# Performance work log

Hardware: AMD Instinct MI355X
Metric: run time of the kernel (lower is better)

Reference implementation:

```python
import jax, jax.numpy as jnp
import numpy as np
from jax import lax

T, I, H = 8192, 1024, 1024


def setup_inputs() -> dict:
    key = jax.random.key(0)
    ks = jax.random.split(key, 7)
    s = 1.0 / np.sqrt(H)
    x = jax.random.normal(ks[0], (T, I), dtype=jnp.float32)
    W_ih = jax.random.uniform(ks[1], (4 * H, I), minval=-s, maxval=s, dtype=jnp.float32)
    W_hh = jax.random.uniform(ks[2], (4 * H, H), minval=-s, maxval=s, dtype=jnp.float32)
    b_ih = jax.random.uniform(ks[3], (4 * H,), minval=-s, maxval=s, dtype=jnp.float32)
    b_hh = jax.random.uniform(ks[4], (4 * H,), minval=-s, maxval=s, dtype=jnp.float32)
    h0 = jax.random.normal(ks[5], (H,), dtype=jnp.float32)
    c0 = jax.random.uniform(ks[6], (H,), dtype=jnp.float32)
    return {"x": x, "W_ih": W_ih, "W_hh": W_hh, "b_ih": b_ih, "b_hh": b_hh, "h0": h0, "c0": c0}


def reference(x, W_ih, W_hh, b_ih, b_hh, h0, c0):
    # Precompute the input contribution to all gates in one big GEMM: [T, 4H]
    gates_x = x @ W_ih.T + (b_ih + b_hh)

    def step(carry, gx):
        h, c = carry
        g = gx + h @ W_hh.T  # [4H]
        i, f, gc, o = jnp.split(g, 4)  # PyTorch gate order: input, forget, cell, output
        i = jax.nn.sigmoid(i)
        f = jax.nn.sigmoid(f)
        gc = jnp.tanh(gc)
        o = jax.nn.sigmoid(o)
        c_new = f * c + i * gc
        h_new = o * jnp.tanh(c_new)
        return (h_new, c_new), h_new

    (_, _), hs = lax.scan(step, (h0, c0), gates_x)
    return hs  # [T, H] — the per-timestep outputs collected in fullDataOutput
```

## Files before the change

### kernel.cpp

```cpp
#include <hip/hip_runtime.h>
#include <cstdint>

#define T_STEPS 8192
#define HDIM 1024

__device__ __forceinline__ float dot4(float4 a, float4 b) {
    return a.x * b.x + a.y * b.y + a.z * b.z + a.w * b.w;
}
__device__ __forceinline__ float sigmoidf_(float x) {
    return 1.0f / (1.0f + __expf(-x));
}
__device__ __forceinline__ float tanhf_(float x) {
    return 1.0f - 2.0f / (__expf(2.0f * x) + 1.0f);
}

__global__ __launch_bounds__(256, 1)
void lstm_persistent(const float* __restrict__ x,
                     const float* __restrict__ W_ih,
                     const float* __restrict__ W_hh,
                     const float* __restrict__ b_ih,
                     const float* __restrict__ b_hh,
                     const float* __restrict__ h0,
                     const float* __restrict__ c0,
                     float* __restrict__ out,
                     unsigned long long* __restrict__ ring)
{
    __shared__ float h_lds[2][HDIM];

    const int tid = threadIdx.x;
    const int w   = tid >> 6;
    const int l   = tid & 63;
    const int u   = blockIdx.x * 4 + w;

    float4 Whh[4][4], Wih[4][4];
#pragma unroll
    for (int q = 0; q < 4; ++q) {
        const float* rh = W_hh + (size_t)(q * HDIM + u) * HDIM;
        const float* ri = W_ih + (size_t)(q * HDIM + u) * HDIM;
#pragma unroll
        for (int i = 0; i < 4; ++i) {
            Whh[q][i] = *(const float4*)(rh + 4 * l + 256 * i);
            Wih[q][i] = *(const float4*)(ri + 4 * l + 256 * i);
        }
    }
    float bias[4];
#pragma unroll
    for (int q = 0; q < 4; ++q) bias[q] = b_ih[q * HDIM + u] + b_hh[q * HDIM + u];
    float c = c0[u];

    float4 hr[4];
#pragma unroll
    for (int i = 0; i < 4; ++i) hr[i] = *(const float4*)(h0 + 4 * l + 256 * i);

    float4 xr[4], xn[4];
#pragma unroll
    for (int i = 0; i < 4; ++i) xr[i] = *(const float4*)(x + 4 * l + 256 * i);
    float gxp[4];
#pragma unroll
    for (int q = 0; q < 4; ++q) {
        float a = 0.f;
#pragma unroll
        for (int i = 0; i < 4; ++i) a += dot4(Wih[q][i], xr[i]);
        gxp[q] = a;
    }
#pragma unroll
    for (int i = 0; i < 4; ++i) xr[i] = *(const float4*)(x + HDIM + 4 * l + 256 * i);

    for (int t = 0; t < T_STEPS; ++t) {
        float acc[4];
#pragma unroll
        for (int q = 0; q < 4; ++q) {
            float a = gxp[q];
#pragma unroll
            for (int i = 0; i < 4; ++i) a += dot4(Whh[q][i], hr[i]);
            acc[q] = a;
        }
#pragma unroll
        for (int m = 1; m < 64; m <<= 1) {
#pragma unroll
            for (int q = 0; q < 4; ++q) acc[q] += __shfl_xor(acc[q], m, 64);
        }
        const float gi = sigmoidf_(acc[0] + bias[0]);
        const float gf = sigmoidf_(acc[1] + bias[1]);
        const float gg = tanhf_   (acc[2] + bias[2]);
        const float go = sigmoidf_(acc[3] + bias[3]);
        c = gf * c + gi * gg;
        const float hval = go * tanhf_(c);

        if (l == 0) {
            out[(size_t)t * HDIM + u] = hval;
            const unsigned long long pk =
                ((unsigned long long)(unsigned)(t + 1) << 32) |
                (unsigned long long)__float_as_uint(hval);
            __hip_atomic_store(&ring[(t & 1) * HDIM + u], pk,
                               __ATOMIC_RELAXED, __HIP_MEMORY_SCOPE_AGENT);
        }
        if (t == T_STEPS - 1) break;

        {
            const int tn = (t + 2 < T_STEPS) ? (t + 2) : (T_STEPS - 1);
            const float* xp = x + (size_t)tn * HDIM;
#pragma unroll
            for (int i = 0; i < 4; ++i) xn[i] = *(const float4*)(xp + 4 * l + 256 * i);
        }
#pragma unroll
        for (int q = 0; q < 4; ++q) {
            float a = 0.f;
#pragma unroll
            for (int i = 0; i < 4; ++i) a += dot4(Wih[q][i], xr[i]);
            gxp[q] = a;
        }

        {
            const unsigned e = (unsigned)(t + 1);
            const unsigned long long* rp = ring + (t & 1) * HDIM + tid;
            unsigned long long v0, v1, v2, v3;
            for (;;) {
                v0 = __hip_atomic_load(rp,       __ATOMIC_RELAXED, __HIP_MEMORY_SCOPE_AGENT);
                v1 = __hip_atomic_load(rp + 256, __ATOMIC_RELAXED, __HIP_MEMORY_SCOPE_AGENT);
                v2 = __hip_atomic_load(rp + 512, __ATOMIC_RELAXED, __HIP_MEMORY_SCOPE_AGENT);
                v3 = __hip_atomic_load(rp + 768, __ATOMIC_RELAXED, __HIP_MEMORY_SCOPE_AGENT);
                if ((unsigned)(v0 >> 32) == e && (unsigned)(v1 >> 32) == e &&
                    (unsigned)(v2 >> 32) == e && (unsigned)(v3 >> 32) == e) break;
                __builtin_amdgcn_s_sleep(1);
            }
            const int ns = (t + 1) & 1;
            h_lds[ns][tid      ] = __uint_as_float((unsigned)v0);
            h_lds[ns][tid + 256] = __uint_as_float((unsigned)v1);
            h_lds[ns][tid + 512] = __uint_as_float((unsigned)v2);
            h_lds[ns][tid + 768] = __uint_as_float((unsigned)v3);
        }
        __syncthreads();
        {
            const int ns = (t + 1) & 1;
#pragma unroll
            for (int i = 0; i < 4; ++i)
                hr[i] = *(const float4*)&h_lds[ns][4 * l + 256 * i];
        }
#pragma unroll
        for (int i = 0; i < 4; ++i) xr[i] = xn[i];
    }
}

extern "C" void kernel_launch(void* const* d_in, const int* in_sizes, int n_in,
                              void* d_out, int out_size, void* d_ws, size_t ws_size,
                              hipStream_t stream)
{
    const float* x    = (const float*)d_in[0];
    const float* W_ih = (const float*)d_in[1];
    const float* W_hh = (const float*)d_in[2];
    const float* b_ih = (const float*)d_in[3];
    const float* b_hh = (const float*)d_in[4];
    const float* h0   = (const float*)d_in[5];
    const float* c0   = (const float*)d_in[6];

    unsigned long long* ring = (unsigned long long*)d_ws;
    hipMemsetAsync(d_ws, 0, 2 * HDIM * sizeof(unsigned long long), stream);
    lstm_persistent<<<256, 256, 0, stream>>>(x, W_ih, W_hh, b_ih, b_hh, h0, c0,
                                             (float*)d_out, ring);
}
```

Measured before the change: 23.61 ms.

## Halve block count, widen blocks, and poll ring with 16-byte uncached loads

The grid goes from 256 blocks of 256 threads to 128 blocks of 512 threads, so each block owns 8 hidden units and fewer blocks take part in the per-step cross-block handshake. The spin-wait now uses one inline-asm global_load_dwordx4 with sc0 sc1 cache bypass per thread, covering two ring entries, instead of four 8-byte atomic loads. The s_sleep backoff is dropped, and the h output store now comes after the ring publish. The risks are heavier memory traffic from tight polling and a 16-byte read of two 8-byte entries that is not guaranteed atomic as a whole, although each entry carries its own step tag.

New measurement: 25.82 ms. 9.4% more time.

```diff
diff --git a/kernel.cpp b/kernel.cpp
--- a/kernel.cpp
+++ b/kernel.cpp
@@ -2,19 +2,27 @@
 #include <cstdint>
 
 #define T_STEPS 8192
-#define HDIM 1024
+#define HDIM    1024
+#define NBLK    128
+#define NTHR    512
+
+typedef unsigned int u32x4 __attribute__((ext_vector_type(4)));
 
 __device__ __forceinline__ float dot4(float4 a, float4 b) {
     return a.x * b.x + a.y * b.y + a.z * b.z + a.w * b.w;
 }
-__device__ __forceinline__ float sigmoidf_(float x) {
-    return 1.0f / (1.0f + __expf(-x));
-}
-__device__ __forceinline__ float tanhf_(float x) {
-    return 1.0f - 2.0f / (__expf(2.0f * x) + 1.0f);
+__device__ __forceinline__ float sigmoidf_(float v) { return 1.0f / (1.0f + __expf(-v)); }
+__device__ __forceinline__ float tanhf_(float v)    { return 1.0f - 2.0f / (__expf(2.0f * v) + 1.0f); }
+
+__device__ __forceinline__ u32x4 poll2(unsigned long long a) {
+    u32x4 r;
+    asm volatile("global_load_dwordx4 %0, %1, off sc0 sc1\n\t"
+                 "s_waitcnt vmcnt(0)"
+                 : "=&v"(r) : "v"(a) : "memory");
+    return r;
 }
 
-__global__ __launch_bounds__(256, 1)
+__global__ __launch_bounds__(NTHR, 2)
 void lstm_persistent(const float* __restrict__ x,
                      const float* __restrict__ W_ih,
                      const float* __restrict__ W_hh,
@@ -30,7 +38,7 @@
     const int tid = threadIdx.x;
     const int w   = tid >> 6;
     const int l   = tid & 63;
-    const int u   = blockIdx.x * 4 + w;
+    const int u   = (blockIdx.x << 3) + w;
 
     float4 Whh[4][4], Wih[4][4];
 #pragma unroll
@@ -52,17 +60,20 @@
 #pragma unroll
     for (int i = 0; i < 4; ++i) hr[i] = *(const float4*)(h0 + 4 * l + 256 * i);
 
+    float gxp[4];
+    {
+        float4 x0[4];
+#pragma unroll
+        for (int i = 0; i < 4; ++i) x0[i] = *(const float4*)(x + 4 * l + 256 * i);
+#pragma unroll
+        for (int q = 0; q < 4; ++q) {
+            float a = 0.f;
+#pragma unroll
+            for (int i = 0; i < 4; ++i) a += dot4(Wih[q][i], x0[i]);
+            gxp[q] = a;
+        }
+    }
     float4 xr[4], xn[4];
-#pragma unroll
-    for (int i = 0; i < 4; ++i) xr[i] = *(const float4*)(x + 4 * l + 256 * i);
-    float gxp[4];
-#pragma unroll
-    for (int q = 0; q < 4; ++q) {
-        float a = 0.f;
-#pragma unroll
-        for (int i = 0; i < 4; ++i) a += dot4(Wih[q][i], xr[i]);
-        gxp[q] = a;
-    }
 #pragma unroll
     for (int i = 0; i < 4; ++i) xr[i] = *(const float4*)(x + HDIM + 4 * l + 256 * i);
 
@@ -88,12 +99,12 @@
         const float hval = go * tanhf_(c);
 
         if (l == 0) {
-            out[(size_t)t * HDIM + u] = hval;
             const unsigned long long pk =
                 ((unsigned long long)(unsigned)(t + 1) << 32) |
                 (unsigned long long)__float_as_uint(hval);
             __hip_atomic_store(&ring[(t & 1) * HDIM + u], pk,
                                __ATOMIC_RELAXED, __HIP_MEMORY_SCOPE_AGENT);
+            out[(size_t)t * HDIM + u] = hval;
         }
         if (t == T_STEPS - 1) break;
 
@@ -113,22 +124,16 @@
 
         {
             const unsigned e = (unsigned)(t + 1);
-            const unsigned long long* rp = ring + (t & 1) * HDIM + tid;
-            unsigned long long v0, v1, v2, v3;
+            const unsigned long long base =
+                (unsigned long long)(ring + (t & 1) * HDIM + 2 * tid);
+            u32x4 p;
             for (;;) {
-                v0 = __hip_atomic_load(rp,       __ATOMIC_RELAXED, __HIP_MEMORY_SCOPE_AGENT);
-                v1 = __hip_atomic_load(rp + 256, __ATOMIC_RELAXED, __HIP_MEMORY_SCOPE_AGENT);
-                v2 = __hip_atomic_load(rp + 512, __ATOMIC_RELAXED, __HIP_MEMORY_SCOPE_AGENT);
-                v3 = __hip_atomic_load(rp + 768, __ATOMIC_RELAXED, __HIP_MEMORY_SCOPE_AGENT);
-                if ((unsigned)(v0 >> 32) == e && (unsigned)(v1 >> 32) == e &&
-                    (unsigned)(v2 >> 32) == e && (unsigned)(v3 >> 32) == e) break;
-                __builtin_amdgcn_s_sleep(1);
+                p = poll2(base);
+                if ((unsigned)p.y == e && (unsigned)p.w == e) break;
             }
             const int ns = (t + 1) & 1;
-            h_lds[ns][tid      ] = __uint_as_float((unsigned)v0);
-            h_lds[ns][tid + 256] = __uint_as_float((unsigned)v1);
-            h_lds[ns][tid + 512] = __uint_as_float((unsigned)v2);
-            h_lds[ns][tid + 768] = __uint_as_float((unsigned)v3);
+            h_lds[ns][2 * tid    ] = __uint_as_float((unsigned)p.x);
+            h_lds[ns][2 * tid + 1] = __uint_as_float((unsigned)p.z);
         }
         __syncthreads();
         {
@@ -156,6 +161,6 @@
 
     unsigned long long* ring = (unsigned long long*)d_ws;
     hipMemsetAsync(d_ws, 0, 2 * HDIM * sizeof(unsigned long long), stream);
-    lstm_persistent<<<256, 256, 0, stream>>>(x, W_ih, W_hh, b_ih, b_hh, h0, c0,
-                                             (float*)d_out, ring);
+    lstm_persistent<<<NBLK, NTHR, 0, stream>>>(x, W_ih, W_hh, b_ih, b_hh, h0, c0,
+                                               (float*)d_out, ring);
 }
```
